# Optimization experiments

Hardware: AMD Instinct MI355X
Metric: run time of the kernel (lower is better)

## Reference

```python
import jax, jax.numpy as jnp
import numpy as np

B, S, D_IN, D_OUT = 4, 2048, 1024, 1024
N_TREES, DEPTH, N_HEADS = 12, 3, 3
N_INTERNAL = 2 ** DEPTH - 1  # 7
N_LEAVES = 2 ** DEPTH        # 8
TEMPERATURE = 1.0
SOFTPLUS_SHIFT = 0.5413      # softplus(0.5413) ~= 1.0, so init node temp ~ 1


def _build_path_indices(depth):
    """Root-to-leaf internal-node indices and go-left directions per leaf."""
    L = 2 ** depth
    pi = np.zeros((L, depth), np.int32)
    pd = np.zeros((L, depth), np.float32)
    for leaf in range(L):
        node = 0
        for d in range(depth):
            pi[leaf, d] = node
            bit = (leaf >> (depth - 1 - d)) & 1
            pd[leaf, d] = 1.0 - bit
            node = 2 * node + 1 + bit
    return pi, pd


def setup_inputs() -> dict:
    key = jax.random.key(0)
    ks = jax.random.split(key, 4)
    x = jax.random.normal(ks[0], (B, S, D_IN), dtype=jnp.float32)
    # normal(0, 0.1) routing init
    decision_weights = 0.1 * jax.random.normal(ks[1], (N_TREES, N_INTERNAL, D_IN), dtype=jnp.float32)
    decision_biases = jnp.zeros((N_TREES, N_INTERNAL), dtype=jnp.float32)
    node_temperature_logits = jnp.zeros((N_TREES, N_INTERNAL), dtype=jnp.float32)
    # nn.Linear default init ~ U(-1/sqrt(D), 1/sqrt(D)); use matching-scale normal
    gate_w = jax.random.normal(ks[2], (N_TREES, D_IN), dtype=jnp.float32) / np.sqrt(D_IN)
    gate_b = jnp.zeros((N_TREES,), dtype=jnp.float32)
    # xavier_normal over each [n_leaves, output_dim] slice
    xav_std = np.sqrt(2.0 / (N_LEAVES + D_OUT))
    leaf_outputs = xav_std * jax.random.normal(ks[3], (N_HEADS, N_TREES, N_LEAVES, D_OUT), dtype=jnp.float32)
    pi, pd = _build_path_indices(DEPTH)
    return {
        "x": x,
        "decision_weights": decision_weights,
        "decision_biases": decision_biases,
        "node_temperature_logits": node_temperature_logits,
        "gate_w": gate_w,
        "gate_b": gate_b,
        "leaf_outputs": leaf_outputs,
        "path_indices": jnp.asarray(pi),
        "path_dirs": jnp.asarray(pd),
    }


def reference(x, decision_weights, decision_biases, node_temperature_logits,
              gate_w, gate_b, leaf_outputs, path_indices, path_dirs):
    # decisions: [B, S, T, N_internal]
    decisions = jnp.einsum('bsd,tnd->bstn', x, decision_weights) + decision_biases
    node_temps = TEMPERATURE * jax.nn.softplus(node_temperature_logits + SOFTPLUS_SHIFT)
    decisions = jax.nn.sigmoid(decisions / node_temps)
    # gather nodes along each root->leaf path: [B, S, T, L, depth]
    relevant = decisions[..., path_indices]
    probs_per_level = path_dirs * relevant + (1.0 - path_dirs) * (1.0 - relevant)
    leaf_probs = probs_per_level.prod(axis=-1)  # [B, S, T, L]
    # softmax gate over trees: [B, S, T]
    weights = jax.nn.softmax(jnp.einsum('bsd,td->bst', x, gate_w) + gate_b, axis=-1)
    # fold tree gate into leaf probs, then contract leaves against leaf outputs
    routed = leaf_probs * weights[..., None]            # [B, S, T, L]
    out = jnp.einsum('bstl,htld->hbsd', routed, leaf_outputs)  # [H, B, S, Dout]
    return out
```

## Files before the change

kernel.cpp:

```cpp
#include <hip/hip_runtime.h>

typedef __attribute__((ext_vector_type(8))) short short8;
typedef __attribute__((ext_vector_type(4))) float floatx4;
typedef unsigned int uint;
typedef unsigned short ushort;
typedef __attribute__((ext_vector_type(4))) uint uintx4;

#define NTOK   8192
#define DIN    1024
#define DOUT   1024
#define NJ     96
#define TOKPB  32
#define XSTR   136
#define DSTR   97
#define SSTR   85
#define LOT_H  (DOUT * NJ)

static __device__ inline ushort f2b(float f) {
    uint u = __builtin_bit_cast(uint, f);
    u = u + 0x7fffu + ((u >> 16) & 1u);
    return (ushort)(u >> 16);
}
static __device__ inline uint pack2(float a, float b) {
    return (uint)f2b(a) | ((uint)f2b(b) << 16);
}

__global__ __launch_bounds__(256) void k_prep(const float* __restrict__ lo,
                                              const float* __restrict__ dw,
                                              const float* __restrict__ gw,
                                              ushort* __restrict__ lot,
                                              ushort* __restrict__ wcat) {
    int i = blockIdx.x * 256 + threadIdx.x;
    if (i < 3 * LOT_H) {
        int h = i / LOT_H;
        int rem = i - h * LOT_H;
        int k = rem >> 10;
        int d = rem & 1023;
        lot[h * LOT_H + d * NJ + k] = f2b(lo[i]);
    } else {
        int j = i - 3 * LOT_H;
        int r = j >> 10, c = j & 1023;
        float v = (r < 84) ? dw[r * DIN + c] : gw[(r - 84) * DIN + c];
        wcat[j] = f2b(v);
    }
}

__global__ __launch_bounds__(256) void k_routed(
    const float* __restrict__ x,
    const ushort* __restrict__ wcat,
    const float* __restrict__ db,
    const float* __restrict__ ntl,
    const float* __restrict__ gb,
    const int*   __restrict__ pi,
    const float* __restrict__ pd,
    ushort* __restrict__ routed)
{
    __shared__ __attribute__((aligned(16))) char smem[34816];
    __shared__ float invt[84];
    __shared__ float biasf[96];
    __shared__ int   pis[24];
    __shared__ float pds[24];

    ushort* xl = (ushort*)smem;
    ushort* wl = (ushort*)(smem + TOKPB * XSTR * 2);
    float*  decis = (float*)smem;
    float*  sdecs = (float*)(smem + TOKPB * DSTR * 4);

    const int tid = threadIdx.x;
    const int tb  = blockIdx.x * TOKPB;

    if (tid < 84) {
        float z = ntl[tid] + 0.5413f;
        float sp = (z > 20.0f) ? z : log1pf(__expf(z));
        invt[tid]  = 1.0f / sp;
        biasf[tid] = db[tid];
    } else if (tid < 96) {
        biasf[tid] = gb[tid - 84];
    } else if (tid < 120) {
        pis[tid - 96] = pi[tid - 96];
    } else if (tid < 144) {
        pds[tid - 120] = pd[tid - 120];
    }

    const int wave = tid >> 6, lane = tid & 63;
    const int lrow = lane & 15, quad = lane >> 4;
    const int wm = wave & 1, wn = wave >> 1;

    floatx4 acc[3];
#pragma unroll
    for (int nt = 0; nt < 3; ++nt) acc[nt] = (floatx4)(0.0f);

    for (int kc = 0; kc < 8; ++kc) {
        __syncthreads();
#pragma unroll
        for (int i = 0; i < 4; ++i) {
            int idx = tid + 256 * i;
            int r = idx >> 5, c = idx & 31;
            float4 v = *(const float4*)(x + (size_t)(tb + r) * DIN + kc * 128 + c * 4);
            uint2 p;
            p.x = pack2(v.x, v.y);
            p.y = pack2(v.z, v.w);
            *(uint2*)(xl + r * XSTR + c * 4) = p;
        }
#pragma unroll
        for (int i = 0; i < 6; ++i) {
            int idx = tid + 256 * i;
            int r = idx >> 4, c = idx & 15;
            uintx4 v = *(const uintx4*)(wcat + r * DIN + kc * 128 + c * 8);
            *(uintx4*)(wl + r * XSTR + c * 8) = v;
        }
        __syncthreads();

        short8 a[4];
#pragma unroll
        for (int kt = 0; kt < 4; ++kt)
            a[kt] = *(const short8*)(xl + (wm * 16 + lrow) * XSTR + kt * 32 + quad * 8);
#pragma unroll
        for (int nt = 0; nt < 3; ++nt) {
#pragma unroll
            for (int kt = 0; kt < 4; ++kt) {
                short8 b = *(const short8*)(wl + (wn * 48 + nt * 16 + lrow) * XSTR + kt * 32 + quad * 8);
                acc[nt] = __builtin_amdgcn_mfma_f32_16x16x32_bf16(a[kt], b, acc[nt], 0, 0, 0);
            }
        }
    }

    __syncthreads();
#pragma unroll
    for (int nt = 0; nt < 3; ++nt)
#pragma unroll
        for (int r = 0; r < 4; ++r)
            decis[(wm * 16 + quad * 4 + r) * DSTR + wn * 48 + nt * 16 + lrow] = acc[nt][r];
    __syncthreads();

#pragma unroll
    for (int i = 0; i < 11; ++i) {
        int idx = tid + 256 * i;
        if (idx < TOKPB * 84) {
            int tk = idx / 84, nd = idx - tk * 84;
            float dv = (decis[tk * DSTR + nd] + biasf[nd]) * invt[nd];
            sdecs[tk * SSTR + nd] = 1.0f / (1.0f + __expf(-dv));
        }
    }
    __syncthreads();

    {
        const int tk = tid >> 3, l = tid & 7;
        float g[12], gm = -1e30f;
#pragma unroll
        for (int tt = 0; tt < 12; ++tt) {
            g[tt] = decis[tk * DSTR + 84 + tt] + biasf[84 + tt];
            gm = fmaxf(gm, g[tt]);
        }
        float gs = 0.0f;
#pragma unroll
        for (int tt = 0; tt < 12; ++tt) { g[tt] = __expf(g[tt] - gm); gs += g[tt]; }
        float ginv = 1.0f / gs;

        const int   n0 = pis[l * 3 + 0], n1 = pis[l * 3 + 1], n2 = pis[l * 3 + 2];
        const float d0 = pds[l * 3 + 0], d1 = pds[l * 3 + 1], d2 = pds[l * 3 + 2];
        const float* sd = sdecs + tk * SSTR;
        ushort* dst = routed + (size_t)(tb + tk) * NJ + l;
#pragma unroll
        for (int t = 0; t < 12; ++t) {
            float s0 = sd[t * 7 + n0], s1 = sd[t * 7 + n1], s2 = sd[t * 7 + n2];
            float pb = g[t] * ginv
                     * (d0 * s0 + (1.0f - d0) * (1.0f - s0))
                     * (d1 * s1 + (1.0f - d1) * (1.0f - s1))
                     * (d2 * s2 + (1.0f - d2) * (1.0f - s2));
            dst[t * 8] = f2b(pb);
        }
    }
}

__global__ __launch_bounds__(256) void k_out(
    const ushort* __restrict__ routed,
    const ushort* __restrict__ lot,
    float* __restrict__ out)
{
    const int tb = blockIdx.x * 64;
    const int d0 = blockIdx.y * 64;
    const int h  = blockIdx.z;
    const int wave = threadIdx.x >> 6, lane = threadIdx.x & 63;
    const int lrow = lane & 15, quad = lane >> 4;

    const ushort* ap = routed + (size_t)(tb + wave * 16 + lrow) * NJ + quad * 8;
    short8 a[3];
#pragma unroll
    for (int kk = 0; kk < 3; ++kk) a[kk] = *(const short8*)(ap + kk * 32);

    const ushort* bp = lot + (size_t)h * LOT_H + (size_t)(d0 + lrow) * NJ + quad * 8;
    floatx4 acc[4];
#pragma unroll
    for (int nt = 0; nt < 4; ++nt) {
        acc[nt] = (floatx4)(0.0f);
#pragma unroll
        for (int kk = 0; kk < 3; ++kk) {
            short8 b = *(const short8*)(bp + nt * 16 * NJ + kk * 32);
            acc[nt] = __builtin_amdgcn_mfma_f32_16x16x32_bf16(a[kk], b, acc[nt], 0, 0, 0);
        }
    }
#pragma unroll
    for (int nt = 0; nt < 4; ++nt) {
        int d = d0 + nt * 16 + lrow;
#pragma unroll
        for (int r = 0; r < 4; ++r) {
            int tok = tb + wave * 16 + quad * 4 + r;
            out[((size_t)h * NTOK + tok) * DOUT + d] = acc[nt][r];
        }
    }
}

extern "C" void kernel_launch(void* const* d_in, const int* in_sizes, int n_in,
                              void* d_out, int out_size, void* d_ws, size_t ws_size,
                              hipStream_t stream) {
    const float* x   = (const float*)d_in[0];
    const float* dw  = (const float*)d_in[1];
    const float* db  = (const float*)d_in[2];
    const float* ntl = (const float*)d_in[3];
    const float* gw  = (const float*)d_in[4];
    const float* gb  = (const float*)d_in[5];
    const float* lo  = (const float*)d_in[6];
    const int*   pi  = (const int*)d_in[7];
    const float* pd  = (const float*)d_in[8];
    float* out = (float*)d_out;

    ushort* routed = (ushort*)d_ws;
    ushort* lot    = routed + (size_t)NTOK * NJ;
    ushort* wcat   = lot + (size_t)3 * LOT_H;

    k_prep<<<dim3((3 * LOT_H + NJ * DIN) / 256), dim3(256), 0, stream>>>(lo, dw, gw, lot, wcat);
    k_routed<<<dim3(NTOK / TOKPB), dim3(256), 0, stream>>>(x, wcat, db, ntl, gb, pi, pd, routed);
    k_out<<<dim3(NTOK / 64, DOUT / 64, 3), dim3(256), 0, stream>>>(routed, lot, out);
}
```

Before: 164.9 us.

## Register-prefetch next K chunk in routing GEMM; widen output tiles with nontemporal stores

The routing kernel now loads the next 128-wide K chunk of x and the weights into registers while the MFMAs on the current chunk run, so global-load latency overlaps compute. x loads are nontemporal. The output kernel doubles each block's D tile to 128 columns, reusing the routed A fragments over more columns and halving the grid, and writes the output with nontemporal stores. The costs are higher register pressure from the prefetch buffers and eight accumulators, and fewer blocks in the output kernel.

```diff
diff --git a/kernel.cpp b/kernel.cpp
--- a/kernel.cpp
+++ b/kernel.cpp
@@ -90,26 +90,52 @@
 #pragma unroll
     for (int nt = 0; nt < 3; ++nt) acc[nt] = (floatx4)(0.0f);
 
+    floatx4 xv[2][4];
+    uintx4  wv[2][6];
+
+#define LOADX(B, KC) do { \
+    _Pragma("unroll") for (int i_ = 0; i_ < 4; ++i_) { \
+        int idx_ = tid + 256 * i_; \
+        int r_ = idx_ >> 5, c_ = idx_ & 31; \
+        xv[B][i_] = __builtin_nontemporal_load( \
+            (const floatx4*)(x + (size_t)(tb + r_) * DIN + (KC) * 128 + c_ * 4)); \
+    } } while (0)
+
+#define LOADW(B, KC) do { \
+    _Pragma("unroll") for (int i_ = 0; i_ < 6; ++i_) { \
+        int idx_ = tid + 256 * i_; \
+        int r_ = idx_ >> 4, c_ = idx_ & 15; \
+        wv[B][i_] = *(const uintx4*)(wcat + r_ * DIN + (KC) * 128 + c_ * 8); \
+    } } while (0)
+
+#define STAGE(B) do { \
+    _Pragma("unroll") for (int i_ = 0; i_ < 4; ++i_) { \
+        int idx_ = tid + 256 * i_; \
+        int r_ = idx_ >> 5, c_ = idx_ & 31; \
+        uint2 p_; \
+        p_.x = pack2(xv[B][i_][0], xv[B][i_][1]); \
+        p_.y = pack2(xv[B][i_][2], xv[B][i_][3]); \
+        *(uint2*)(xl + r_ * XSTR + c_ * 4) = p_; \
+    } \
+    _Pragma("unroll") for (int i_ = 0; i_ < 6; ++i_) { \
+        int idx_ = tid + 256 * i_; \
+        int r_ = idx_ >> 4, c_ = idx_ & 15; \
+        *(uintx4*)(wl + r_ * XSTR + c_ * 8) = wv[B][i_]; \
+    } } while (0)
+
+    LOADX(0, 0);
+    LOADW(0, 0);
+
+#pragma unroll
     for (int kc = 0; kc < 8; ++kc) {
+        const int cur = kc & 1, nxt = cur ^ 1;
         __syncthreads();
-#pragma unroll
-        for (int i = 0; i < 4; ++i) {
-            int idx = tid + 256 * i;
-            int r = idx >> 5, c = idx & 31;
-            float4 v = *(const float4*)(x + (size_t)(tb + r) * DIN + kc * 128 + c * 4);
-            uint2 p;
-            p.x = pack2(v.x, v.y);
-            p.y = pack2(v.z, v.w);
-            *(uint2*)(xl + r * XSTR + c * 4) = p;
-        }
-#pragma unroll
-        for (int i = 0; i < 6; ++i) {
-            int idx = tid + 256 * i;
-            int r = idx >> 4, c = idx & 15;
-            uintx4 v = *(const uintx4*)(wcat + r * DIN + kc * 128 + c * 8);
-            *(uintx4*)(wl + r * XSTR + c * 8) = v;
-        }
+        STAGE(cur);
         __syncthreads();
+        if (kc < 7) {
+            LOADX(nxt, kc + 1);
+            LOADW(nxt, kc + 1);
+        }
 
         short8 a[4];
 #pragma unroll
@@ -124,6 +150,9 @@
             }
         }
     }
+#undef LOADX
+#undef LOADW
+#undef STAGE
 
     __syncthreads();
 #pragma unroll
@@ -179,7 +208,7 @@
     float* __restrict__ out)
 {
     const int tb = blockIdx.x * 64;
-    const int d0 = blockIdx.y * 64;
+    const int d0 = blockIdx.y * 128;
     const int h  = blockIdx.z;
     const int wave = threadIdx.x >> 6, lane = threadIdx.x & 63;
     const int lrow = lane & 15, quad = lane >> 4;
@@ -190,9 +219,9 @@
     for (int kk = 0; kk < 3; ++kk) a[kk] = *(const short8*)(ap + kk * 32);
 
     const ushort* bp = lot + (size_t)h * LOT_H + (size_t)(d0 + lrow) * NJ + quad * 8;
-    floatx4 acc[4];
-#pragma unroll
-    for (int nt = 0; nt < 4; ++nt) {
+    floatx4 acc[8];
+#pragma unroll
+    for (int nt = 0; nt < 8; ++nt) {
         acc[nt] = (floatx4)(0.0f);
 #pragma unroll
         for (int kk = 0; kk < 3; ++kk) {
@@ -201,12 +230,13 @@
         }
     }
 #pragma unroll
-    for (int nt = 0; nt < 4; ++nt) {
+    for (int nt = 0; nt < 8; ++nt) {
         int d = d0 + nt * 16 + lrow;
 #pragma unroll
         for (int r = 0; r < 4; ++r) {
             int tok = tb + wave * 16 + quad * 4 + r;
-            out[((size_t)h * NTOK + tok) * DOUT + d] = acc[nt][r];
+            __builtin_nontemporal_store(acc[nt][r],
+                out + ((size_t)h * NTOK + tok) * DOUT + d);
         }
     }
 }
@@ -231,5 +261,5 @@
 
     k_prep<<<dim3((3 * LOT_H + NJ * DIN) / 256), dim3(256), 0, stream>>>(lo, dw, gw, lot, wcat);
     k_routed<<<dim3(NTOK / TOKPB), dim3(256), 0, stream>>>(x, wcat, db, ntl, gb, pi, pd, routed);
-    k_out<<<dim3(NTOK / 64, DOUT / 64, 3), dim3(256), 0, stream>>>(routed, lot, out);
-}
+    k_out<<<dim3(NTOK / 64, DOUT / 128, 3), dim3(256), 0, stream>>>(routed, lot, out);
+}
```

Result: slower. 174.1 us (+5.6%).
